# Kernel optimization log

Hardware: AMD Instinct MI355X
Metric: run time of the kernel (lower is better)

Reference implementation:

```python
import jax, jax.numpy as jnp
import numpy as np

WINDOW = 60
DEPTH = 3
HIDDEN = 256
LN_EPS = 1e-5


def _lyndon_indices(d):
    # Lyndon words over alphabet {0..d-1}, lengths 2 and 3, lexicographic order
    # (signatory mode='words' extracts expanded-logsig coefficients at Lyndon words).
    i2 = np.array([(i, j) for i in range(d) for j in range(d) if (i, j) < (j, i)], dtype=np.int32)
    i3 = np.array([(i, j, k) for i in range(d) for j in range(d) for k in range(d)
                   if (i, j, k) < (j, k, i) and (i, j, k) < (k, i, j)], dtype=np.int32)
    return i2, i3


def _logsig_features(x):
    # x: [b, s, c] -> logsignature of time-augmented sliding windows: [b*s, sig_channels]
    b, s, c = x.shape
    d = c + 1
    # replicate-padded sliding windows via clipped gather (matches F.pad replicate + unfold)
    pos = jnp.clip(jnp.arange(s)[:, None] + jnp.arange(WINDOW)[None, :] - (WINDOW - 1), 0, s - 1)
    windows = x[:, pos, :]                                   # [b, s, W, c]
    t = jnp.linspace(0.0, 1.0, WINDOW, dtype=x.dtype)        # time augmentation channel
    t_b = jnp.broadcast_to(t[None, None, :, None], (b, s, WINDOW, 1))
    aug = jnp.concatenate([t_b, windows], axis=-1).reshape(b * s, WINDOW, d)
    N = b * s
    # basepoint=True: prepend zero point -> increments include the first point itself
    inc = jnp.diff(aug, axis=1, prepend=jnp.zeros((N, 1, d), aug.dtype))  # [N, W, d]
    inc_t = jnp.transpose(inc, (1, 0, 2))                    # [W, N, d]

    def chen_step(carry, v):
        S1, S2, S3 = carry
        vv = jnp.einsum('ni,nj->nij', v, v)
        vvv = jnp.einsum('nij,nk->nijk', vv, v)
        nS3 = S3 + jnp.einsum('nij,nk->nijk', S2, v) \
                 + 0.5 * jnp.einsum('ni,njk->nijk', S1, vv) + vvv / 6.0
        nS2 = S2 + jnp.einsum('ni,nj->nij', S1, v) + 0.5 * vv
        nS1 = S1 + v
        return (nS1, nS2, nS3), None

    init = (jnp.zeros((N, d), x.dtype), jnp.zeros((N, d, d), x.dtype), jnp.zeros((N, d, d, d), x.dtype))
    (S1, S2, S3), _ = jax.lax.scan(chen_step, init, inc_t)
    # log in truncated tensor algebra: log(1+x) = x - x^2/2 + x^3/3
    L1 = S1
    L2 = S2 - 0.5 * jnp.einsum('ni,nj->nij', S1, S1)
    L3 = (S3 - 0.5 * (jnp.einsum('ni,njk->nijk', S1, S2) + jnp.einsum('nij,nk->nijk', S2, S1))
          + jnp.einsum('ni,nj,nk->nijk', S1, S1, S1) / 3.0)
    i2, i3 = _lyndon_indices(d)
    f2 = L2[:, i2[:, 0], i2[:, 1]]
    f3 = L3[:, i3[:, 0], i3[:, 1], i3[:, 2]]
    return jnp.concatenate([L1, f2, f3], axis=-1)            # [N, sig_channels]


def setup_inputs() -> dict:
    key = jax.random.key(0)
    ks = jax.random.split(key, 5)
    b, s, c = 8, 2048, 8
    d = c + 1
    sig_channels = d + (d * d - d) // 2 + (d ** 3 - d) // 3  # 285 for d=9
    h2 = 2 * HIDDEN
    x = jax.random.normal(ks[0], (b, s, c), dtype=jnp.float32)
    w1 = jax.random.normal(ks[1], (sig_channels, h2), dtype=jnp.float32) / np.sqrt(sig_channels)
    b1 = jnp.zeros((h2,), jnp.float32)
    ln_g = jnp.ones((h2,), jnp.float32)
    ln_b = jnp.zeros((h2,), jnp.float32)
    w2 = jax.random.normal(ks[2], (h2, HIDDEN), dtype=jnp.float32) / np.sqrt(h2)
    b2 = jnp.zeros((HIDDEN,), jnp.float32)
    return {"x": x, "w1": w1, "b1": b1, "ln_g": ln_g, "ln_b": ln_b, "w2": w2, "b2": b2}


def reference(x, w1, b1, ln_g, ln_b, w2, b2):
    b, s, _ = x.shape
    feats = _logsig_features(x)                              # [b*s, sig_channels]
    h = jax.nn.gelu(feats @ w1 + b1, approximate=False)      # torch default GELU (erf)
    mu = jnp.mean(h, axis=-1, keepdims=True)
    var = jnp.var(h, axis=-1, keepdims=True)
    h = (h - mu) / jnp.sqrt(var + LN_EPS) * ln_g + ln_b      # LayerNorm; Dropout is eval no-op
    out = h @ w2 + b2
    return out.reshape(b, s, -1)
```

## Files before the change

### kernel.cpp

```cpp
#include <hip/hip_runtime.h>
#include <hip/hip_bf16.h>
#include <cstdint>
#include <cstddef>

typedef short short8 __attribute__((ext_vector_type(8)));
typedef float f32x4 __attribute__((ext_vector_type(4)));
typedef float f32x2 __attribute__((ext_vector_type(2)));

#define NS    2048
#define KPAD  288
#define H2    512
#define HID   256
#define WPB   7
#define SBLK  293

#define MFMA(a,b,c) __builtin_amdgcn_mfma_f32_16x16x32_bf16((a),(b),(c),0,0,0)

__device__ __forceinline__ void gl2lds16(const void* g, void* l) {
    __builtin_amdgcn_global_load_lds(
        (const __attribute__((address_space(1))) void*)g,
        (__attribute__((address_space(3))) void*)l, 16, 0, 0);
}
__device__ __forceinline__ float geluf(float x) {
    return 0.5f * x * (1.0f + erff(x * 0.70710678118654752f));
}
__device__ __forceinline__ f32x4 shfl4(f32x4 v, int d) {
    f32x4 r;
    r[0] = __shfl_xor(v[0], d); r[1] = __shfl_xor(v[1], d);
    r[2] = __shfl_xor(v[2], d); r[3] = __shfl_xor(v[3], d);
    return r;
}

struct Tbl3 { short col[729]; };
static constexpr Tbl3 make_tbl3() {
    Tbl3 t{};
    for (int x = 0; x < 729; ++x) t.col[x] = -1;
    int r = 0;
    for (int i = 0; i < 9; ++i)
        for (int j = 0; j < 9; ++j)
            for (int k = 0; k < 9; ++k) {
                bool lt1 = (i < j) || (i == j && (j < k || (j == k && k < i)));
                bool lt2 = (i < k) || (i == k && (j < i || (j == i && k < j)));
                if (lt1 && lt2) { t.col[(i*9+j)*9+k] = (short)(45 + r); ++r; }
            }
    return t;
}
static constexpr Tbl3 TBL3 = make_tbl3();

#define SIG_STEP(VA_,VB_,VC_) { \
    const float hh = 0.5f * S1i + vi * (1.0f/6.0f); \
    const float ra = S2ra + hh * (VA_); \
    const float rb = S2rb + hh * (VB_); \
    const float rc = S2rc + hh * (VC_); \
    const f32x2 ra2 = {ra, ra}, rb2 = {rb, rb}, rc2 = {rc, rc}; \
    S3sa += ra * v0; S3pa0 += ra2*vp0; S3pa1 += ra2*vp1; S3pa2 += ra2*vp2; S3pa3 += ra2*vp3; \
    S3sb += rb * v0; S3pb0 += rb2*vp0; S3pb1 += rb2*vp1; S3pb2 += rb2*vp2; S3pb3 += rb2*vp3; \
    S3sc += rc * v0; S3pc0 += rc2*vp0; S3pc1 += rc2*vp1; S3pc2 += rc2*vp2; S3pc3 += rc2*vp3; \
    const float aa = S1i + 0.5f * vi; \
    S2ra += aa * (VA_); S2rb += aa * (VB_); S2rc += aa * (VC_); \
    S1i += vi; }

#define SIG_MAIN(VA_,VB_,VC_) { \
    { const float* xr = &X[(g0 - lo) * 8]; \
      const float4 e0 = *(const float4*)xr; \
      const float4 e1 = *(const float4*)(xr + 4); \
      const float rs = xr[ioff]; \
      const float v0 = 0.0f; \
      const f32x2 vp0 = {e0.x, e0.y}, vp1 = {e0.z, e0.w}, vp2 = {e1.x, e1.y}, vp3 = {e1.z, e1.w}; \
      const float vi = (ci == 0) ? 0.0f : rs; \
      SIG_STEP(VA_,VB_,VC_) } \
    const float* pd = &PD[(sm59 + 1 - lo + 59) * 8]; \
    float4 d0 = *(const float4*)pd; \
    float4 d1 = *(const float4*)(pd + 4); \
    float rn = pd[ioff]; \
    _Pragma("unroll 2") \
    for (int j = 1; j < 60; ++j) { \
      const float4 e0 = d0; const float4 e1 = d1; const float rs = rn; \
      pd += 8; \
      d0 = *(const float4*)pd; d1 = *(const float4*)(pd + 4); rn = pd[ioff]; \
      const float v0 = DT; \
      const f32x2 vp0 = {e0.x, e0.y}, vp1 = {e0.z, e0.w}, vp2 = {e1.x, e1.y}, vp3 = {e1.z, e1.w}; \
      const float vi = (ci == 0) ? DT : rs; \
      SIG_STEP(VA_,VB_,VC_) \
    } }

#define SIG_ST(RA,RB,RC) \
    if (act) { \
        if ((RA) == 0) S1buf[widx * 9 + ci] = S1i; \
        float* sb = &S2buf[widx * 81 + ci * 9]; \
        sb[RA] = S2ra; sb[RB] = S2rb; sb[RC] = S2rc; \
    }

#define S3EL0(SL) S3s##SL
#define S3EL1(SL) S3p##SL##0[0]
#define S3EL2(SL) S3p##SL##0[1]
#define S3EL3(SL) S3p##SL##1[0]
#define S3EL4(SL) S3p##SL##1[1]
#define S3EL5(SL) S3p##SL##2[0]
#define S3EL6(SL) S3p##SL##2[1]
#define S3EL7(SL) S3p##SL##3[0]
#define S3EL8(SL) S3p##SL##3[1]

#define SIG_E2(SL,J2) if (ci < (J2)) { \
    const float val2 = S2r##SL - 0.5f * S1i * s1v##J2; \
    const int col2 = 9 + ci*8 - (ci*(ci-1))/2 + ((J2) - ci - 1); \
    frow[col2] = __float2bfloat16(val2); }

#define SIG_E3(SL,R,K) { const int col3 = TBL3.col[tb + (R)*9 + (K)]; \
    if (col3 >= 0) { \
        const float val3 = S3EL##K(SL) \
            - 0.5f * (S1i * S2w[(R)*9+(K)] + S2r##SL * s1v##K) \
            + S1i * s1v##R * s1v##K * (1.0f/3.0f); \
        frow[col3] = __float2bfloat16(val3); } }

#define SIG_E3R(SL,R) SIG_E3(SL,R,0) SIG_E3(SL,R,1) SIG_E3(SL,R,2) SIG_E3(SL,R,3) \
    SIG_E3(SL,R,4) SIG_E3(SL,R,5) SIG_E3(SL,R,6) SIG_E3(SL,R,7) SIG_E3(SL,R,8)

#define SIG_EMIT(RA,RB,RC) \
    if (act) { \
        if ((RA) == 0) { \
            frow[ci] = __float2bfloat16(S1i); \
            if (ci == 0) { \
                const __hip_bfloat16 z16 = __float2bfloat16(0.0f); \
                frow[285] = z16; frow[286] = z16; frow[287] = z16; \
            } \
        } \
        SIG_E2(a,RA) SIG_E2(b,RB) SIG_E2(c,RC) \
        SIG_E3R(a,RA) SIG_E3R(b,RB) SIG_E3R(c,RC) \
    }

__global__ __launch_bounds__(192) __attribute__((amdgpu_waves_per_eu(1, 6)))
void sig_kernel(const float* __restrict__ x, __hip_bfloat16* __restrict__ feats) {
    __shared__ __align__(16) float X[66 * 8];
    __shared__ __align__(16) float PD[126 * 8];
    __shared__ float S2buf[WPB * 81];
    __shared__ float S1buf[WPB * 9];

    const int blk = blockIdx.x;
    const int b   = blk / SBLK;
    const int s0  = (blk % SBLK) * WPB;
    const int lo  = (s0 - 59 > 0) ? (s0 - 59) : 0;
    const int hi  = (s0 + WPB - 1 < NS - 1) ? (s0 + WPB - 1) : (NS - 1);
    const int nrow = hi - lo + 1;
    const int tid = threadIdx.x;

    {
        const float4* src = (const float4*)(x + ((size_t)b * NS + lo) * 8);
        float4* X4 = (float4*)X;
        const int n4 = nrow * 2;
        for (int t = tid; t < n4; t += 192) X4[t] = src[t];
    }
    __syncthreads();
    {
        const float4* X4 = (const float4*)X;
        float4* PD4 = (float4*)PD;
        for (int t = tid; t < 252; t += 192) {
            const int p = t >> 1;
            const int r = p - 59;
            float4 dv = {0.f, 0.f, 0.f, 0.f};
            if (r > 0 && r < nrow) {
                const float4 a = X4[t - 118], bb = X4[t - 120];
                dv.x = a.x - bb.x; dv.y = a.y - bb.y; dv.z = a.z - bb.z; dv.w = a.w - bb.w;
            }
            PD4[t] = dv;
        }
    }
    __syncthreads();

    const int t3    = tid >> 6;
    const int lt    = tid & 63;
    const int widx0 = lt / 9;
    const int ci    = lt - widx0 * 9;
    const bool act  = (lt < 63) && (s0 + widx0 < NS);
    const int widx  = (widx0 < WPB - 1) ? widx0 : WPB - 1;
    int s = s0 + widx; if (s > NS - 1) s = NS - 1;

    float S3sa=0.f, S3sb=0.f, S3sc=0.f;
    f32x2 S3pa0={0.f,0.f},S3pa1={0.f,0.f},S3pa2={0.f,0.f},S3pa3={0.f,0.f};
    f32x2 S3pb0={0.f,0.f},S3pb1={0.f,0.f},S3pb2={0.f,0.f},S3pb3={0.f,0.f};
    f32x2 S3pc0={0.f,0.f},S3pc1={0.f,0.f},S3pc2={0.f,0.f},S3pc3={0.f,0.f};
    float S2ra=0.f, S2rb=0.f, S2rc=0.f;
    float S1i = 0.f;
    const int ioff = (ci > 0) ? (ci - 1) : 0;
    const int sm59 = s - 59;
    const int g0   = (sm59 > 0) ? sm59 : 0;
    const float DT = 1.0f / 59.0f;

    if (t3 == 0)      { SIG_MAIN(v0,   e0.x, e0.y) }
    else if (t3 == 1) { SIG_MAIN(e0.z, e0.w, e1.x) }
    else              { SIG_MAIN(e1.y, e1.z, e1.w) }

    if (t3 == 0)      { SIG_ST(0,1,2) }
    else if (t3 == 1) { SIG_ST(3,4,5) }
    else              { SIG_ST(6,7,8) }
    __syncthreads();

    const float* s1p = &S1buf[widx * 9];
    const float s1v0=s1p[0], s1v1=s1p[1], s1v2=s1p[2], s1v3=s1p[3], s1v4=s1p[4];
    const float s1v5=s1p[5], s1v6=s1p[6], s1v7=s1p[7], s1v8=s1p[8];
    const float* S2w = &S2buf[widx * 81];
    const int tb = ci * 81;
    __hip_bfloat16* frow = feats + (size_t)(b * NS + s) * KPAD;

    if (t3 == 0)      { SIG_EMIT(0,1,2) }
    else if (t3 == 1) { SIG_EMIT(3,4,5) }
    else              { SIG_EMIT(6,7,8) }
}

__global__ __launch_bounds__(512)
void prep_kernel(const float* __restrict__ w1, const float* __restrict__ w2,
                 const float* __restrict__ lng, const float* __restrict__ lnb,
                 const float* __restrict__ b2,
                 __hip_bfloat16* __restrict__ w1T, __hip_bfloat16* __restrict__ w2g,
                 float* __restrict__ gw, float* __restrict__ cvec) {
    const int blk = blockIdx.x;
    if (blk < 256) {
        const int n = blk, k = threadIdx.x;
        const float wv = w2[(size_t)k * HID + n];
        const float a = lng[k] * wv;
        const float c = lnb[k] * wv;
        w2g[(size_t)n * H2 + k] = __float2bfloat16(a);
        float ra = a, rc = c;
#pragma unroll
        for (int d = 1; d < 64; d <<= 1) { ra += __shfl_xor(ra, d); rc += __shfl_xor(rc, d); }
        __shared__ float r1[8], r2[8];
        const int wv_ = k >> 6, ln = k & 63;
        if (ln == 0) { r1[wv_] = ra; r2[wv_] = rc; }
        __syncthreads();
        if (k == 0) {
            float sa = 0.f, sc = 0.f;
#pragma unroll
            for (int i = 0; i < 8; ++i) { sa += r1[i]; sc += r2[i]; }
            gw[n] = sa; cvec[n] = sc + b2[n];
        }
    } else {
        const int n = blk - 256;
        const int k = threadIdx.x;
        if (k < KPAD) {
            const float v = (k < 285) ? w1[(size_t)k * H2 + n] : 0.0f;
            w1T[(size_t)n * KPAD + k] = __float2bfloat16(v);
        }
    }
}

__global__ __launch_bounds__(256)
void mlp_kernel(const __hip_bfloat16* __restrict__ feats,
                const __hip_bfloat16* __restrict__ w1T,
                const float* __restrict__ bias,
                const __hip_bfloat16* __restrict__ w2g,
                const float* __restrict__ gw,
                const float* __restrict__ cvec,
                float* __restrict__ out) {
    __shared__ __align__(16) __hip_bfloat16 Blds[512 * 32];
    __shared__ __align__(16) __hip_bfloat16 Hbuf[32 * 512];
    __shared__ __align__(16) __hip_bfloat16 Ab0[32 * 32];
    __shared__ __align__(16) __hip_bfloat16 Ab1[32 * 32];
    __shared__ float sstat[4][32][2];

    const int tid  = threadIdx.x;
    const int wave = tid >> 6;
    const int lane = tid & 63;
    const int quad = lane >> 4;
    const int l16  = lane & 15;
    const int m0   = blockIdx.x * 32;
    const int swz16 = (quad ^ ((l16 >> 1) & 3)) * 16;

#define STAGE_B1(S, DST) { \
    _Pragma("unroll") \
    for (int i_ = 0; i_ < 8; ++i_) { \
        const int c_ = tid + i_ * 256; const int r_ = c_ >> 2; const int q_ = c_ & 3; \
        gl2lds16(w1T + (size_t)r_ * KPAD + (S) * 32 + ((q_ ^ ((r_ >> 1) & 3)) * 8), \
                 (char*)(DST) + (c_ & ~63) * 16); } }
#define STAGE_A(S, DST) { if (tid < 128) { \
        const int r_ = tid >> 2; const int q_ = tid & 3; \
        gl2lds16(feats + (size_t)(m0 + r_) * KPAD + (S) * 32 + ((q_ ^ ((r_ >> 1) & 3)) * 8), \
                 (char*)(DST) + (tid & ~63) * 16); } }
#define STAGE_B2(T, DST) { \
    _Pragma("unroll") \
    for (int i_ = 0; i_ < 4; ++i_) { \
        const int c_ = tid + i_ * 256; const int r_ = c_ >> 2; const int q_ = c_ & 3; \
        gl2lds16(w2g + (size_t)r_ * H2 + (T) * 32 + ((q_ ^ ((r_ >> 1) & 3)) * 8), \
                 (char*)(DST) + (c_ & ~63) * 16); } }

    ((float*)sstat)[tid] = 0.0f;
    STAGE_B1(0, Blds)
    STAGE_A(0, Ab0)
    __syncthreads();

    f32x4 a1[2][8];
#pragma unroll
    for (int mf = 0; mf < 2; ++mf)
#pragma unroll
        for (int nf = 0; nf < 8; ++nf) a1[mf][nf] = f32x4{0.f, 0.f, 0.f, 0.f};

#pragma unroll 1
    for (int s = 0; s < 9; ++s) {
        if (s < 8) {
            if ((s + 1) & 1) { STAGE_B1(s + 1, Hbuf) STAGE_A(s + 1, Ab1) }
            else             { STAGE_B1(s + 1, Blds) STAGE_A(s + 1, Ab0) }
        }
        const char* Ac = (s & 1) ? (const char*)Ab1 : (const char*)Ab0;
        const char* Bc = (s & 1) ? (const char*)Hbuf : (const char*)Blds;
        const short8 av0 = *(const short8*)(Ac + l16 * 64 + swz16);
        const short8 av1 = *(const short8*)(Ac + (16 + l16) * 64 + swz16);
#pragma unroll
        for (int nf = 0; nf < 8; ++nf) {
            const short8 bv = *(const short8*)(Bc + (size_t)(wave * 128 + nf * 16 + l16) * 64 + swz16);
            a1[0][nf] = MFMA(av0, bv, a1[0][nf]);
            a1[1][nf] = MFMA(av1, bv, a1[1][nf]);
        }
        __syncthreads();
    }

    {
        f32x4 sum0 = {0,0,0,0}, sum1 = {0,0,0,0}, sq0 = {0,0,0,0}, sq1 = {0,0,0,0};
#pragma unroll
        for (int nf = 0; nf < 8; ++nf) {
            const int col = wave * 128 + nf * 16 + l16;
            const float bv = bias[col];
            f32x4 e0, e1;
#pragma unroll
            for (int r = 0; r < 4; ++r) { e0[r] = geluf(a1[0][nf][r] + bv); e1[r] = geluf(a1[1][nf][r] + bv); }
#pragma unroll
            for (int r = 0; r < 4; ++r) {
                const int row0 = quad * 4 + r;
                const int row1 = 16 + row0;
                const int ch0 = (col >> 3) ^ (row0 & 7);
                const int ch1 = (col >> 3) ^ (row1 & 7);
                *(__hip_bfloat16*)((char*)Hbuf + row0 * 1024 + ch0 * 16 + (col & 7) * 2) = __float2bfloat16(e0[r]);
                *(__hip_bfloat16*)((char*)Hbuf + row1 * 1024 + ch1 * 16 + (col & 7) * 2) = __float2bfloat16(e1[r]);
            }
            sum0 += e0; sq0 += e0 * e0; sum1 += e1; sq1 += e1 * e1;
        }
        sum0 += shfl4(sum0, 1); sq0 += shfl4(sq0, 1); sum1 += shfl4(sum1, 1); sq1 += shfl4(sq1, 1);
        sum0 += shfl4(sum0, 2); sq0 += shfl4(sq0, 2); sum1 += shfl4(sum1, 2); sq1 += shfl4(sq1, 2);
        sum0 += shfl4(sum0, 4); sq0 += shfl4(sq0, 4); sum1 += shfl4(sum1, 4); sq1 += shfl4(sq1, 4);
        sum0 += shfl4(sum0, 8); sq0 += shfl4(sq0, 8); sum1 += shfl4(sum1, 8); sq1 += shfl4(sq1, 8);
        if (l16 == 0) {
#pragma unroll
            for (int r = 0; r < 4; ++r) {
                sstat[wave][quad * 4 + r][0]      = sum0[r];
                sstat[wave][quad * 4 + r][1]      = sq0[r];
                sstat[wave][16 + quad * 4 + r][0] = sum1[r];
                sstat[wave][16 + quad * 4 + r][1] = sq1[r];
            }
        }
        __syncthreads();
    }

    f32x4 a2[2][4];
#pragma unroll
    for (int mf = 0; mf < 2; ++mf)
#pragma unroll
        for (int nf = 0; nf < 4; ++nf) a2[mf][nf] = f32x4{0.f, 0.f, 0.f, 0.f};

    STAGE_B2(0, Blds)
    __syncthreads();

    const int hsw = l16 & 7;
#pragma unroll 1
    for (int t = 0; t < 16; ++t) {
        if (t < 15) { STAGE_B2(t + 1, (char*)Blds + ((t + 1) & 1) * 16384) }
        const char* Bc = (const char*)Blds + (t & 1) * 16384;
        const int kc = ((t * 4 + quad) ^ hsw) * 16;
        const short8 hv0 = *(const short8*)((const char*)Hbuf + l16 * 1024 + kc);
        const short8 hv1 = *(const short8*)((const char*)Hbuf + (16 + l16) * 1024 + kc);
#pragma unroll
        for (int nf = 0; nf < 4; ++nf) {
            const short8 bv = *(const short8*)(Bc + (size_t)(wave * 64 + nf * 16 + l16) * 64 + swz16);
            a2[0][nf] = MFMA(hv0, bv, a2[0][nf]);
            a2[1][nf] = MFMA(hv1, bv, a2[1][nf]);
        }
        __syncthreads();
    }

    f32x4 mu0, rs0, mu1, rs1;
#pragma unroll
    for (int r = 0; r < 4; ++r) {
        const int rl0 = quad * 4 + r, rl1 = 16 + rl0;
        const float s0 = sstat[0][rl0][0] + sstat[1][rl0][0] + sstat[2][rl0][0] + sstat[3][rl0][0];
        const float q0 = sstat[0][rl0][1] + sstat[1][rl0][1] + sstat[2][rl0][1] + sstat[3][rl0][1];
        const float s1 = sstat[0][rl1][0] + sstat[1][rl1][0] + sstat[2][rl1][0] + sstat[3][rl1][0];
        const float q1 = sstat[0][rl1][1] + sstat[1][rl1][1] + sstat[2][rl1][1] + sstat[3][rl1][1];
        mu0[r] = s0 * (1.0f / 512.0f);
        mu1[r] = s1 * (1.0f / 512.0f);
        rs0[r] = rsqrtf(q0 * (1.0f / 512.0f) - mu0[r] * mu0[r] + 1e-5f);
        rs1[r] = rsqrtf(q1 * (1.0f / 512.0f) - mu1[r] * mu1[r] + 1e-5f);
    }
#pragma unroll
    for (int nf = 0; nf < 4; ++nf) {
        const int col = wave * 64 + nf * 16 + l16;
        const float g_ = gw[col], c_ = cvec[col];
#pragma unroll
        for (int r = 0; r < 4; ++r) {
            const int row0 = m0 + quad * 4 + r;
            const int row1 = row0 + 16;
            out[(size_t)row0 * HID + col] = rs0[r] * (a2[0][nf][r] - mu0[r] * g_) + c_;
            out[(size_t)row1 * HID + col] = rs1[r] * (a2[1][nf][r] - mu1[r] * g_) + c_;
        }
    }
}

extern "C" void kernel_launch(void* const* d_in, const int* in_sizes, int n_in,
                              void* d_out, int out_size, void* d_ws, size_t ws_size,
                              hipStream_t stream) {
    const float* x   = (const float*)d_in[0];
    const float* w1  = (const float*)d_in[1];
    const float* b1  = (const float*)d_in[2];
    const float* lng = (const float*)d_in[3];
    const float* lnb = (const float*)d_in[4];
    const float* w2  = (const float*)d_in[5];
    const float* b2  = (const float*)d_in[6];
    float* out = (float*)d_out;

    char* ws = (char*)d_ws;
    __hip_bfloat16* feats = (__hip_bfloat16*)(ws);
    __hip_bfloat16* w1T   = (__hip_bfloat16*)(ws + 9437184);
    __hip_bfloat16* w2g   = (__hip_bfloat16*)(ws + 9732096);
    float*          gw    = (float*)(ws + 9994240);
    float*          cvec  = (float*)(ws + 9995264);

    prep_kernel<<<dim3(768), dim3(512), 0, stream>>>(w1, w2, lng, lnb, b2,
                                                     w1T, w2g, gw, cvec);
    sig_kernel<<<dim3(8 * SBLK), dim3(192), 0, stream>>>(x, feats);
    mlp_kernel<<<dim3(512), dim3(256), 0, stream>>>(feats, w1T, b1, w2g, gw, cvec, out);
}
```

Baseline: 149.8 us.

## Compute two adjacent sliding-window signatures per thread sharing increment loads

Each thread now handles two consecutive windows (s and s+1), so each block covers 14 windows instead of 7 and launches half as many blocks. Inside the Chen loop, each increment row loaded from LDS is used for window A at step j and reused for window B at step j-1, which halves the LDS loads per signature step. The cost is about twice as many accumulator registers, which lowers occupancy since the waves_per_eu hint was dropped, and a serialized emit phase that runs twice per thread.

```diff
diff --git a/kernel.cpp b/kernel.cpp
--- a/kernel.cpp
+++ b/kernel.cpp
@@ -11,8 +11,8 @@
 #define KPAD  288
 #define H2    512
 #define HID   256
-#define WPB   7
-#define SBLK  293
+#define WPB2  14
+#define SBLK2 147
 
 #define MFMA(a,b,c) __builtin_amdgcn_mfma_f32_16x16x32_bf16((a),(b),(c),0,0,0)
 
@@ -47,48 +47,62 @@
 }
 static constexpr Tbl3 TBL3 = make_tbl3();
 
-#define SIG_STEP(VA_,VB_,VC_) { \
-    const float hh = 0.5f * S1i + vi * (1.0f/6.0f); \
-    const float ra = S2ra + hh * (VA_); \
-    const float rb = S2rb + hh * (VB_); \
-    const float rc = S2rc + hh * (VC_); \
+#define SIG_STEPX(P,VA_,VB_,VC_) { \
+    const float hh = 0.5f * S1i##P + vi * (1.0f/6.0f); \
+    const float ra = S2ra##P + hh * (VA_); \
+    const float rb = S2rb##P + hh * (VB_); \
+    const float rc = S2rc##P + hh * (VC_); \
     const f32x2 ra2 = {ra, ra}, rb2 = {rb, rb}, rc2 = {rc, rc}; \
-    S3sa += ra * v0; S3pa0 += ra2*vp0; S3pa1 += ra2*vp1; S3pa2 += ra2*vp2; S3pa3 += ra2*vp3; \
-    S3sb += rb * v0; S3pb0 += rb2*vp0; S3pb1 += rb2*vp1; S3pb2 += rb2*vp2; S3pb3 += rb2*vp3; \
-    S3sc += rc * v0; S3pc0 += rc2*vp0; S3pc1 += rc2*vp1; S3pc2 += rc2*vp2; S3pc3 += rc2*vp3; \
-    const float aa = S1i + 0.5f * vi; \
-    S2ra += aa * (VA_); S2rb += aa * (VB_); S2rc += aa * (VC_); \
-    S1i += vi; }
-
-#define SIG_MAIN(VA_,VB_,VC_) { \
-    { const float* xr = &X[(g0 - lo) * 8]; \
-      const float4 e0 = *(const float4*)xr; \
-      const float4 e1 = *(const float4*)(xr + 4); \
-      const float rs = xr[ioff]; \
-      const float v0 = 0.0f; \
-      const f32x2 vp0 = {e0.x, e0.y}, vp1 = {e0.z, e0.w}, vp2 = {e1.x, e1.y}, vp3 = {e1.z, e1.w}; \
-      const float vi = (ci == 0) ? 0.0f : rs; \
-      SIG_STEP(VA_,VB_,VC_) } \
-    const float* pd = &PD[(sm59 + 1 - lo + 59) * 8]; \
-    float4 d0 = *(const float4*)pd; \
-    float4 d1 = *(const float4*)(pd + 4); \
-    float rn = pd[ioff]; \
-    _Pragma("unroll 2") \
+    S3sa##P += ra * v0; S3pa0##P += ra2*vp0; S3pa1##P += ra2*vp1; S3pa2##P += ra2*vp2; S3pa3##P += ra2*vp3; \
+    S3sb##P += rb * v0; S3pb0##P += rb2*vp0; S3pb1##P += rb2*vp1; S3pb2##P += rb2*vp2; S3pb3##P += rb2*vp3; \
+    S3sc##P += rc * v0; S3pc0##P += rc2*vp0; S3pc1##P += rc2*vp1; S3pc2##P += rc2*vp2; S3pc3##P += rc2*vp3; \
+    const float aa = S1i##P + 0.5f * vi; \
+    S2ra##P += aa * (VA_); S2rb##P += aa * (VB_); S2rc##P += aa * (VC_); \
+    S1i##P += vi; }
+
+#define SIG_SEED(P, G0, VA_,VB_,VC_) { \
+    const float* xr = &X[((G0) - lo) * 8]; \
+    const float4 e0 = *(const float4*)xr; \
+    const float4 e1 = *(const float4*)(xr + 4); \
+    const float rs = xr[ioff]; \
+    const float v0 = 0.0f; \
+    const f32x2 vp0 = {e0.x, e0.y}, vp1 = {e0.z, e0.w}, vp2 = {e1.x, e1.y}, vp3 = {e1.z, e1.w}; \
+    const float vi = (ci == 0) ? 0.0f : rs; \
+    SIG_STEPX(P, VA_,VB_,VC_) }
+
+#define SIG_MAIN2(VA_,VB_,VC_) { \
+    SIG_SEED(, g0A, VA_,VB_,VC_) \
+    SIG_SEED(B, g0B, VA_,VB_,VC_) \
+    const float* pd = &PD[(sA - 58 - lo + 59) * 8]; \
+    float4 p0 = *(const float4*)pd; \
+    float4 p1 = *(const float4*)(pd + 4); \
+    float pr = pd[ioff]; \
+    _Pragma("unroll 1") \
     for (int j = 1; j < 60; ++j) { \
-      const float4 e0 = d0; const float4 e1 = d1; const float rs = rn; \
       pd += 8; \
-      d0 = *(const float4*)pd; d1 = *(const float4*)(pd + 4); rn = pd[ioff]; \
-      const float v0 = DT; \
-      const f32x2 vp0 = {e0.x, e0.y}, vp1 = {e0.z, e0.w}, vp2 = {e1.x, e1.y}, vp3 = {e1.z, e1.w}; \
-      const float vi = (ci == 0) ? DT : rs; \
-      SIG_STEP(VA_,VB_,VC_) \
+      const float4 c0 = *(const float4*)pd; \
+      const float4 c1 = *(const float4*)(pd + 4); \
+      const float cr = pd[ioff]; \
+      { const float4 e0 = p0; const float4 e1 = p1; const float rs = pr; \
+        const float v0 = DT; \
+        const f32x2 vp0 = {e0.x, e0.y}, vp1 = {e0.z, e0.w}, vp2 = {e1.x, e1.y}, vp3 = {e1.z, e1.w}; \
+        const float vi = (ci == 0) ? DT : rs; \
+        SIG_STEPX(, VA_,VB_,VC_) } \
+      { const float4 e0 = c0; const float4 e1 = c1; const float rs = cr; \
+        const float v0 = DT; \
+        const f32x2 vp0 = {e0.x, e0.y}, vp1 = {e0.z, e0.w}, vp2 = {e1.x, e1.y}, vp3 = {e1.z, e1.w}; \
+        const float vi = (ci == 0) ? DT : rs; \
+        SIG_STEPX(B, VA_,VB_,VC_) } \
+      p0 = c0; p1 = c1; pr = cr; \
     } }
 
-#define SIG_ST(RA,RB,RC) \
-    if (act) { \
-        if ((RA) == 0) S1buf[widx * 9 + ci] = S1i; \
-        float* sb = &S2buf[widx * 81 + ci * 9]; \
-        sb[RA] = S2ra; sb[RB] = S2rb; sb[RC] = S2rc; \
+#define SIG_ST2(RA,RB,RC) \
+    if (lt < 63) { \
+        if ((RA) == 0) { S1buf[(2*widx)*9 + ci] = S1i; S1buf[(2*widx+1)*9 + ci] = S1iB; } \
+        float* sa_ = &S2buf[(2*widx)*81 + ci*9]; \
+        sa_[RA] = S2ra;  sa_[RB] = S2rb;  sa_[RC] = S2rc; \
+        float* sb_ = &S2buf[(2*widx+1)*81 + ci*9]; \
+        sb_[RA] = S2raB; sb_[RB] = S2rbB; sb_[RC] = S2rcB; \
     }
 
 #define S3EL0(SL) S3s##SL
@@ -129,18 +143,30 @@
         SIG_E3R(a,RA) SIG_E3R(b,RB) SIG_E3R(c,RC) \
     }
 
-__global__ __launch_bounds__(192) __attribute__((amdgpu_waves_per_eu(1, 6)))
+#define SIG_EMIT_W(SLOT, SVAL, ACT) { \
+    const bool act = (ACT); \
+    const float* s1p = &S1buf[(SLOT) * 9]; \
+    const float s1v0=s1p[0], s1v1=s1p[1], s1v2=s1p[2], s1v3=s1p[3], s1v4=s1p[4]; \
+    const float s1v5=s1p[5], s1v6=s1p[6], s1v7=s1p[7], s1v8=s1p[8]; \
+    const float* S2w = &S2buf[(SLOT) * 81]; \
+    const int tb = ci * 81; \
+    __hip_bfloat16* frow = feats + (size_t)(b * NS + (SVAL)) * KPAD; \
+    if (t3 == 0)      { SIG_EMIT(0,1,2) } \
+    else if (t3 == 1) { SIG_EMIT(3,4,5) } \
+    else              { SIG_EMIT(6,7,8) } }
+
+__global__ __launch_bounds__(192)
 void sig_kernel(const float* __restrict__ x, __hip_bfloat16* __restrict__ feats) {
-    __shared__ __align__(16) float X[66 * 8];
-    __shared__ __align__(16) float PD[126 * 8];
-    __shared__ float S2buf[WPB * 81];
-    __shared__ float S1buf[WPB * 9];
+    __shared__ __align__(16) float X[73 * 8];
+    __shared__ __align__(16) float PD[132 * 8];
+    __shared__ float S2buf[WPB2 * 81];
+    __shared__ float S1buf[WPB2 * 9];
 
     const int blk = blockIdx.x;
-    const int b   = blk / SBLK;
-    const int s0  = (blk % SBLK) * WPB;
+    const int b   = blk / SBLK2;
+    const int s0  = (blk % SBLK2) * WPB2;
     const int lo  = (s0 - 59 > 0) ? (s0 - 59) : 0;
-    const int hi  = (s0 + WPB - 1 < NS - 1) ? (s0 + WPB - 1) : (NS - 1);
+    const int hi  = (s0 + WPB2 - 1 < NS - 1) ? (s0 + WPB2 - 1) : (NS - 1);
     const int nrow = hi - lo + 1;
     const int tid = threadIdx.x;
 
@@ -154,7 +180,8 @@
     {
         const float4* X4 = (const float4*)X;
         float4* PD4 = (float4*)PD;
-        for (int t = tid; t < 252; t += 192) {
+        const int tot = (59 + nrow) * 2;
+        for (int t = tid; t < tot; t += 192) {
             const int p = t >> 1;
             const int r = p - 59;
             float4 dv = {0.f, 0.f, 0.f, 0.f};
@@ -171,9 +198,13 @@
     const int lt    = tid & 63;
     const int widx0 = lt / 9;
     const int ci    = lt - widx0 * 9;
-    const bool act  = (lt < 63) && (s0 + widx0 < NS);
-    const int widx  = (widx0 < WPB - 1) ? widx0 : WPB - 1;
-    int s = s0 + widx; if (s > NS - 1) s = NS - 1;
+    const int widx  = (widx0 < 7) ? widx0 : 6;
+
+    int sA = s0 + 2 * widx;
+    const bool actA = (lt < 63) && (sA < NS);
+    const bool actB = (lt < 63) && (sA + 1 < NS);
+    if (sA > NS - 2) sA = NS - 2;
+    const int sB = sA + 1;
 
     float S3sa=0.f, S3sb=0.f, S3sc=0.f;
     f32x2 S3pa0={0.f,0.f},S3pa1={0.f,0.f},S3pa2={0.f,0.f},S3pa3={0.f,0.f};
@@ -181,30 +212,35 @@
     f32x2 S3pc0={0.f,0.f},S3pc1={0.f,0.f},S3pc2={0.f,0.f},S3pc3={0.f,0.f};
     float S2ra=0.f, S2rb=0.f, S2rc=0.f;
     float S1i = 0.f;
+    float S3saB=0.f, S3sbB=0.f, S3scB=0.f;
+    f32x2 S3pa0B={0.f,0.f},S3pa1B={0.f,0.f},S3pa2B={0.f,0.f},S3pa3B={0.f,0.f};
+    f32x2 S3pb0B={0.f,0.f},S3pb1B={0.f,0.f},S3pb2B={0.f,0.f},S3pb3B={0.f,0.f};
+    f32x2 S3pc0B={0.f,0.f},S3pc1B={0.f,0.f},S3pc2B={0.f,0.f},S3pc3B={0.f,0.f};
+    float S2raB=0.f, S2rbB=0.f, S2rcB=0.f;
+    float S1iB = 0.f;
+
     const int ioff = (ci > 0) ? (ci - 1) : 0;
-    const int sm59 = s - 59;
-    const int g0   = (sm59 > 0) ? sm59 : 0;
+    const int g0A  = (sA - 59 > 0) ? (sA - 59) : 0;
+    const int g0B  = (sB - 59 > 0) ? (sB - 59) : 0;
     const float DT = 1.0f / 59.0f;
 
-    if (t3 == 0)      { SIG_MAIN(v0,   e0.x, e0.y) }
-    else if (t3 == 1) { SIG_MAIN(e0.z, e0.w, e1.x) }
-    else              { SIG_MAIN(e1.y, e1.z, e1.w) }
-
-    if (t3 == 0)      { SIG_ST(0,1,2) }
-    else if (t3 == 1) { SIG_ST(3,4,5) }
-    else              { SIG_ST(6,7,8) }
+    if (t3 == 0)      { SIG_MAIN2(v0,   e0.x, e0.y) }
+    else if (t3 == 1) { SIG_MAIN2(e0.z, e0.w, e1.x) }
+    else              { SIG_MAIN2(e1.y, e1.z, e1.w) }
+
+    if (t3 == 0)      { SIG_ST2(0,1,2) }
+    else if (t3 == 1) { SIG_ST2(3,4,5) }
+    else              { SIG_ST2(6,7,8) }
     __syncthreads();
 
-    const float* s1p = &S1buf[widx * 9];
-    const float s1v0=s1p[0], s1v1=s1p[1], s1v2=s1p[2], s1v3=s1p[3], s1v4=s1p[4];
-    const float s1v5=s1p[5], s1v6=s1p[6], s1v7=s1p[7], s1v8=s1p[8];
-    const float* S2w = &S2buf[widx * 81];
-    const int tb = ci * 81;
-    __hip_bfloat16* frow = feats + (size_t)(b * NS + s) * KPAD;
-
-    if (t3 == 0)      { SIG_EMIT(0,1,2) }
-    else if (t3 == 1) { SIG_EMIT(3,4,5) }
-    else              { SIG_EMIT(6,7,8) }
+    SIG_EMIT_W(2 * widx, sA, actA)
+
+    S1i = S1iB; S2ra = S2raB; S2rb = S2rbB; S2rc = S2rcB;
+    S3sa = S3saB; S3sb = S3sbB; S3sc = S3scB;
+    S3pa0 = S3pa0B; S3pa1 = S3pa1B; S3pa2 = S3pa2B; S3pa3 = S3pa3B;
+    S3pb0 = S3pb0B; S3pb1 = S3pb1B; S3pb2 = S3pb2B; S3pb3 = S3pb3B;
+    S3pc0 = S3pc0B; S3pc1 = S3pc1B; S3pc2 = S3pc2B; S3pc3 = S3pc3B;
+    SIG_EMIT_W(2 * widx + 1, sB, actB)
 }
 
 __global__ __launch_bounds__(512)
@@ -422,6 +458,6 @@
 
     prep_kernel<<<dim3(768), dim3(512), 0, stream>>>(w1, w2, lng, lnb, b2,
                                                      w1T, w2g, gw, cvec);
-    sig_kernel<<<dim3(8 * SBLK), dim3(192), 0, stream>>>(x, feats);
+    sig_kernel<<<dim3(8 * SBLK2), dim3(192), 0, stream>>>(x, feats);
     mlp_kernel<<<dim3(512), dim3(256), 0, stream>>>(feats, w1T, b1, w2g, gw, cvec, out);
 }
```

Result: slower. 153.2 us (+2.3%).
